# Optimization experiments

Hardware: AMD Instinct MI355X
Metric: run time of the kernel (lower is better)

Reference implementation:

```python
import jax, jax.numpy as jnp
import numpy as np
from jax import lax

L = 32          # lattice side
H = 128         # net_width / hidden_size
B = 512         # batch_size
EPS = 1e-8


def setup_inputs() -> dict:
    key = jax.random.key(0)
    k0, k1, k2, k3, k4 = jax.random.split(key, 5)
    # binary spin configurations in {0., 1.}
    samples = jnp.round(jax.random.uniform(k0, (B, L, L))).astype(jnp.float32)
    s1 = 1.0 / np.sqrt(H + 2)
    # per-cell linear1 weights: input = cat([x(2), h(H)]) -> H
    W1 = jax.random.uniform(k1, (L * L, H, H + 2), minval=-s1, maxval=s1, dtype=jnp.float32)
    b1 = jax.random.uniform(k2, (L * L, H), minval=-s1, maxval=s1, dtype=jnp.float32)
    sf = 1.0 / np.sqrt(H)
    # per-cell fc head: H -> 1
    Wf = jax.random.uniform(k3, (L * L, H), minval=-sf, maxval=sf, dtype=jnp.float32)
    bf = jax.random.uniform(k4, (L * L,), minval=-sf, maxval=sf, dtype=jnp.float32)
    return {"samples": samples, "W1": W1, "b1": b1, "Wf": Wf, "bf": bf}


def _log_prob(samples, W1, b1, Wf, bf):
    Bsz = samples.shape[0]
    dt = samples.dtype
    W1 = W1.reshape(L, L, H, H + 2)
    b1 = b1.reshape(L, L, H)
    Wf = Wf.reshape(L, L, H)
    bf = bf.reshape(L, L)

    rows = jnp.transpose(samples, (1, 0, 2))                       # (L, B, L)
    prev = jnp.concatenate([jnp.zeros((1, Bsz, L), dt), rows[:-1]], axis=0)  # row above (x_v); zeros for row 0
    parity = (jnp.arange(L) % 2) == 1                              # odd rows scan right-to-left (zigzag)

    def row_step(h_v, xs):
        cur, pv, p, Wr, br, wfr, bfr = xs
        # reorder everything into visitation order (reverse for odd rows)
        cur_o = jnp.where(p, cur[:, ::-1], cur)     # (B, L) current-row spins / mask
        pv_o = jnp.where(p, pv[:, ::-1], pv)        # (B, L) spins of row above (x_v)
        hv_o = jnp.where(p, h_v[::-1], h_v)         # (L, B, H) vertical hidden states
        Wr_o = jnp.where(p, Wr[::-1], Wr)
        br_o = jnp.where(p, br[::-1], br)
        wf_o = jnp.where(p, wfr[::-1], wfr)
        bf_o = jnp.where(p, bfr[::-1], bfr)
        # horizontal input x_h = previously visited spin in this row (0 at row start)
        xh = jnp.concatenate([jnp.zeros((Bsz, 1), dt), cur_o[:, :-1]], axis=1)  # (B, L)

        def cell(h_h, cxs):
            xh_j, xv_j, m_j, hv_j, W, b, wf, bfs = cxs
            xh_s = jnp.stack([xh_j, 1.0 - xh_j], axis=1)   # (B, 2)
            xv_s = jnp.stack([xv_j, 1.0 - xv_j], axis=1)   # (B, 2)
            # linear1 applied to both (x_h,h_h) and (x_v,h_v); linear2 is unused in the original forward
            inp = jnp.concatenate([xh_s, h_h], axis=1) + jnp.concatenate([xv_s, hv_j], axis=1)  # (B, H+2)
            h = jnp.tanh(inp @ W.T + 2.0 * b)              # (B, H)
            x_hat = jax.nn.sigmoid(h @ wf + bfs)           # (B,)
            lp = jnp.log(x_hat + EPS) * m_j + jnp.log(1.0 - x_hat + EPS) * (1.0 - m_j)
            return h, (h, lp)

        cxs = (xh.T, pv_o.T, cur_o.T, hv_o, Wr_o, br_o, wf_o, bf_o)
        _, (hs, lps) = lax.scan(cell, jnp.zeros((Bsz, H), dt), cxs)
        h_v_new = jnp.where(p, hs[::-1], hs)               # back to raw column order
        return h_v_new, lps.sum(axis=0)                    # (B,) row log-prob

    h_v0 = jnp.zeros((L, Bsz, H), dt)
    _, row_lps = lax.scan(row_step, h_v0, (rows, prev, parity, W1, b1, Wf, bf))
    return row_lps.sum(axis=0)                             # (B,)


def reference(samples, W1, b1, Wf, bf):
    return _log_prob(samples, W1, b1, Wf, bf)
```

## Files before the change

### kernel.cpp

```cpp
#include <hip/hip_runtime.h>
#include <math.h>
#include <stdint.h>

#define Lr 32
#define Hh 128
#define NCELL (Lr * Lr)
#define NEPS 1e-8f
#define CELLB 33792

typedef _Float16 f16;
typedef f16 h2 __attribute__((ext_vector_type(2)));
typedef uint32_t u32;
typedef u32 u32x4 __attribute__((ext_vector_type(4)));
typedef u32 u32x2 __attribute__((ext_vector_type(2)));

__device__ __forceinline__ void bar_lds() {
    asm volatile("s_waitcnt lgkmcnt(0)\n\ts_barrier" ::: "memory");
}

template<int CTRL>
__device__ __forceinline__ float dpp_get(float x) {
    return __int_as_float(__builtin_amdgcn_update_dpp(
        0, __float_as_int(x), CTRL, 0xf, 0xf, true));
}

__device__ __forceinline__ float rlane(float x, int l) {
    return __int_as_float(__builtin_amdgcn_readlane(__float_as_int(x), l));
}

__device__ __forceinline__ float dot2(h2 a, h2 b, float c) {
    return __builtin_amdgcn_fdot2(a, b, c, false);
}

__device__ __forceinline__ h2 bch2(u32 v) {
    union { u32 u; h2 h; } cv; cv.u = v; return cv.h;
}
__device__ __forceinline__ float h16(u32 w, int hi) {
    union { unsigned short u; f16 h; } c;
    c.u = (unsigned short)(hi ? (w >> 16) : (w & 0xffff));
    return (float)c.h;
}

__device__ __forceinline__ float fast_tanh(float x) {
    x = fminf(9.f, fmaxf(-9.f, x));
    const float e = __expf(2.f * x);
    return 1.f - 2.f / (e + 1.f);
}

__device__ __forceinline__ int cell_of(int s) {
    const int i = s >> 5, jj = s & 31;
    const int c = (i & 1) ? (Lr - 1 - jj) : jj;
    return i * Lr + c;
}

__global__ __launch_bounds__(256)
void transpose_w(const float* __restrict__ W1, const float* __restrict__ b1,
                 const float* __restrict__ Wf, char* __restrict__ Wt) {
    __shared__ float tile[Hh * 130];
    const int cell = blockIdx.x;
    const float* src = W1 + (size_t)cell * (Hh * 130);
    for (int idx = threadIdx.x; idx < Hh * 130; idx += 256)
        tile[idx] = src[idx];
    __syncthreads();
    char* dst = Wt + (size_t)cell * CELLB;
    const int t = threadIdx.x;
    for (int idx = t; idx < 2048; idx += 256) {
        const int c4 = idx >> 9, tt = idx & 511;
        const int kk = tt >> 2, q = tt & 3;
        union { u32x4 v; f16 h[8]; } o;
        for (int j = 0; j < 4; ++j) {
            const int p = q * 16 + c4 * 4 + j;
            o.h[2 * j]     = (f16)tile[kk * 130 + 2 + 2 * p];
            o.h[2 * j + 1] = (f16)tile[kk * 130 + 3 + 2 * p];
        }
        *(u32x4*)(dst + c4 * 8192 + tt * 16) = o.v;
    }
    if (t < Hh) {
        union { u32x2 v; f16 h[4]; } o;
        const float w0 = tile[t * 130 + 0], w1 = tile[t * 130 + 1];
        const float bb = 2.f * b1[cell * Hh + t];
        o.h[0] = (f16)(2.f * w1 + bb);
        o.h[1] = (f16)(w0 + w1 + bb);
        o.h[2] = (f16)(2.f * w0 + bb);
        o.h[3] = (f16)Wf[cell * Hh + t];
        *(u32x2*)(dst + 32768 + t * 8) = o.v;
    }
}

__global__ __launch_bounds__(512, 4)
void rnn2d(const float* __restrict__ samples,
           const char* __restrict__ Wt,
           const float* __restrict__ bfv,
           float* __restrict__ out)
{
    __shared__ __align__(16) h2  inp[2][64];
    __shared__ __align__(16) f16 hvh[Lr * Hh];
    __shared__ float smp[NCELL];
    __shared__ float bfs[NCELL];
    __shared__ __align__(16) float fp_[2][8];
    __shared__ int   sidx[2];
    __shared__ float lpb[2];

    const int t = threadIdx.x;
    const int k = t >> 2;
    const int q = t & 3;
    const int w = t >> 6;
    const int b = blockIdx.x;

    u32 vc[4], vt;
    for (int c4 = 0; c4 < 4; ++c4) vc[c4] = (u32)(c4 * 8192 + t * 16);
    vt = (u32)(32768 + k * 8);

    {
        f16* z1 = (f16*)inp;
        for (int idx = t; idx < 2 * 64 * 2; idx += 512) z1[idx] = (f16)0.f;
        f16* z2 = (f16*)hvh;
        for (int idx = t; idx < Lr * Hh; idx += 512) z2[idx] = (f16)0.f;
        for (int idx = t; idx < NCELL; idx += 512) {
            smp[idx] = samples[(size_t)b * NCELL + idx];
            bfs[idx] = bfv[idx];
        }
        if (t == 0) sidx[0] = 0;
    }
    float lp = 0.f;

    u32x4 A0,A1,A2,A3, B0,B1,B2,B3, C0,C1,C2,C3, D0,D1,D2,D3;
    u32x2 TA, TB, TC, TD;

#define ISSUE(S, W0,W1_,W2_,W3_, TT)                                        \
    {                                                                       \
        const int s_ = ((S) < NCELL) ? (S) : 0;   \
        const char* cb_ = Wt + (size_t)cell_of(s_) * CELLB;                 \
        asm volatile("global_load_dwordx4 %0, %1, %2" : "=v"(W0)  : "v"(vc[0]), "s"(cb_)); \
        asm volatile("global_load_dwordx4 %0, %1, %2" : "=v"(W1_) : "v"(vc[1]), "s"(cb_)); \
        asm volatile("global_load_dwordx4 %0, %1, %2" : "=v"(W2_) : "v"(vc[2]), "s"(cb_)); \
        asm volatile("global_load_dwordx4 %0, %1, %2" : "=v"(W3_) : "v"(vc[3]), "s"(cb_)); \
        asm volatile("global_load_dwordx2 %0, %1, %2" : "=v"(TT)  : "v"(vt),    "s"(cb_)); \
    }

#define WAITP()                                                             \
    asm volatile("s_waitcnt vmcnt(10)" ::: "memory");                       \
    __builtin_amdgcn_sched_barrier(0);

#define DOT4(WQ, QQ, C4)                                                    \
    {                                                                       \
        const u32x4 v_ = (WQ);                                              \
        const uint4 xa_ = *(const uint4*)&inp[QQ][q * 16 + (C4) * 4];       \
        a00 = dot2(bch2(v_.x), bch2(xa_.x), a00);                           \
        a01 = dot2(bch2(v_.y), bch2(xa_.y), a01);                           \
        a02 = dot2(bch2(v_.z), bch2(xa_.z), a02);                           \
        a03 = dot2(bch2(v_.w), bch2(xa_.w), a03);                           \
    }

#define PROC(S, Q, W0,W1_,W2_,W3_, TT)                                      \
    {                                                                       \
        const int i_ = (S) >> 5, j_ = (S) & 31;                             \
        const int c_ = (i_ & 1) ? (Lr - 1 - j_) : j_;                       \
        const int sn_ = ((S) + 1 < NCELL) ? (S) + 1 : (S);                  \
        const int in_ = sn_ >> 5, jn_ = sn_ & 31;                           \
        const int cn_ = (in_ & 1) ? (Lr - 1 - jn_) : jn_;                   \
        const float hvn = (float)hvh[cn_ * Hh + k];                         \
           \
                       \
        if (((t & 63) == 4) && (w == 4 || w == 5) && (S) > 0) {             \
            const int cp_ = cell_of((S) - 1);                               \
            const float4 fa_ = *(const float4*)&fp_[Q][0];                  \
            const float4 fb_ = *(const float4*)&fp_[Q][4];                  \
            const float z_ = ((fa_.x + fa_.y) + (fa_.z + fa_.w))            \
                           + ((fb_.x + fb_.y) + (fb_.z + fb_.w)) + bfs[cp_];\
            const float xh_ = 1.f / (1.f + __expf(-z_));                    \
            const float m_ = smp[cp_];                                      \
            lp += (w == 4) ? __logf(xh_ + NEPS) * m_                        \
                           : __logf(1.f - xh_ + NEPS) * (1.f - m_);         \
        }                                                                   \
           \
        float a00 = 0.f, a01 = 0.f, a02 = 0.f, a03 = 0.f;                   \
        DOT4(W0,  Q, 0) DOT4(W1_, Q, 1)                                     \
        DOT4(W2_, Q, 2) DOT4(W3_, Q, 3)                                     \
        float s0 = (a00 + a01) + (a02 + a03);                               \
        s0 += dpp_get<0xB1>(s0);                    \
        s0 += dpp_get<0x4E>(s0);   \
                     \
        const int sx = sidx[Q];                                             \
        const float t0_ = h16(TT.x, 0), t1_ = h16(TT.x, 1);                 \
        const float t2_ = h16(TT.y, 0), wfv = h16(TT.y, 1);                 \
        s0 += (sx == 2) ? t2_ : ((sx == 1) ? t1_ : t0_);                    \
        const float h0 = fast_tanh(s0);                                     \
            \
           \
        float f0 = h0 * wfv;                                                \
        f0 += dpp_get<0x141>(f0);                                           \
        f0 += dpp_get<0x140>(f0);                                           \
        f0 = f0 + rlane(f0, 16) + rlane(f0, 32) + rlane(f0, 48);            \
        if ((S) + 1 < NCELL) {                                              \
            const float v0 = ((jn_ == 0) ? 0.f : h0)                        \
                           + ((cn_ == c_) ? h0 : hvn);                      \
            const float v0p = __shfl_down(v0, 4);    \
            if ((t & 7) == 0) {                                             \
                h2 u0; u0.x = (f16)v0; u0.y = (f16)v0p;                     \
                inp[(Q) ^ 1][t >> 3] = u0;                                  \
            }                                                               \
            if (t == 0) {                                                   \
                const float xh0 = (jn_ == 0) ? 0.f : smp[i_ * Lr + c_];     \
                const float xv0 = (in_ == 0) ? 0.f                          \
                                             : smp[(in_ - 1) * Lr + cn_];   \
                sidx[(Q) ^ 1] = (int)(xh0 + xv0);                           \
            }                                                               \
        }                                                                   \
        if ((t & 3) == 0) hvh[c_ * Hh + k] = (f16)h0;    \
        if ((t & 63) == 0) fp_[(Q) ^ 1][w] = f0;                            \
        bar_lds();        \
    }

    ISSUE(0, A0,A1,A2,A3, TA);
    ISSUE(1, B0,B1,B2,B3, TB);
    __syncthreads();

    for (int s = 0; s < NCELL; s += 4) {
        ISSUE(s + 2, C0,C1,C2,C3, TC); WAITP();
        PROC(s,     0, A0,A1,A2,A3, TA);
        ISSUE(s + 3, D0,D1,D2,D3, TD); WAITP();
        PROC(s + 1, 1, B0,B1,B2,B3, TB);
        ISSUE(s + 4, A0,A1,A2,A3, TA); WAITP();
        PROC(s + 2, 0, C0,C1,C2,C3, TC);
        ISSUE(s + 5, B0,B1,B2,B3, TB); WAITP();
        PROC(s + 3, 1, D0,D1,D2,D3, TD);
    }
#undef ISSUE
#undef WAITP
#undef DOT4
#undef PROC

    if (((t & 63) == 4) && (w == 4 || w == 5)) {
        const int cp_ = cell_of(NCELL - 1);
        const float4 fa_ = *(const float4*)&fp_[0][0];
        const float4 fb_ = *(const float4*)&fp_[0][4];
        const float z_ = ((fa_.x + fa_.y) + (fa_.z + fa_.w))
                       + ((fb_.x + fb_.y) + (fb_.z + fb_.w)) + bfs[cp_];
        const float xh_ = 1.f / (1.f + __expf(-z_));
        const float m_ = smp[cp_];
        lp += (w == 4) ? __logf(xh_ + NEPS) * m_
                       : __logf(1.f - xh_ + NEPS) * (1.f - m_);
        lpb[w - 4] = lp;
    }
    __syncthreads();
    if (t == 0) out[b] = lpb[0] + lpb[1];
}

extern "C" void kernel_launch(void* const* d_in, const int* in_sizes, int n_in,
                              void* d_out, int out_size, void* d_ws, size_t ws_size,
                              hipStream_t stream) {
    const float* samples = (const float*)d_in[0];
    const float* W1      = (const float*)d_in[1];
    const float* b1      = (const float*)d_in[2];
    const float* Wf      = (const float*)d_in[3];
    const float* bf      = (const float*)d_in[4];
    float* outp = (float*)d_out;
    char* Wt = (char*)d_ws;

    transpose_w<<<1024, 256, 0, stream>>>(W1, b1, Wf, Wt);
    rnn2d<<<512, 512, 0, stream>>>(samples, Wt, bf, outp);
}
```

Baseline: 1.040 ms.

## Batch 16 samples per block and compute cell matvec with MFMA

The kernel used to run one block per sample, doing a 128x128 fp16 dot2 matvec per cell. Each block now handles 16 batch elements and computes the per-cell product as a 128x16 matrix multiply with 16x16x32 f16 MFMA instructions. Weights are re-laid out in the transpose kernel to match the MFMA A-operand fragments, and samples are bit-packed into per-cell masks. Each weight fetch is now reused across 16 samples, which cuts global weight traffic 16x. The cost is only 32 blocks, so far fewer CUs are busy and the serial chain of cells may become latency bound, and the per-element vertical hidden state takes a large LDS buffer.

Measured after the change: 1.222 ms. 1.17x slower.

```diff
diff --git a/kernel.cpp b/kernel.cpp
--- a/kernel.cpp
+++ b/kernel.cpp
@@ -7,46 +7,33 @@
 #define NCELL (Lr * Lr)
 #define NEPS 1e-8f
 #define CELLB 33792
+#define ELEMS 16
 
 typedef _Float16 f16;
-typedef f16 h2 __attribute__((ext_vector_type(2)));
+typedef f16 f16x4 __attribute__((ext_vector_type(4)));
+typedef f16 f16x8 __attribute__((ext_vector_type(8)));
+typedef float f32x4 __attribute__((ext_vector_type(4)));
 typedef uint32_t u32;
+typedef u32 u32x2 __attribute__((ext_vector_type(2)));
 typedef u32 u32x4 __attribute__((ext_vector_type(4)));
-typedef u32 u32x2 __attribute__((ext_vector_type(2)));
 
 __device__ __forceinline__ void bar_lds() {
     asm volatile("s_waitcnt lgkmcnt(0)\n\ts_barrier" ::: "memory");
 }
 
-template<int CTRL>
-__device__ __forceinline__ float dpp_get(float x) {
-    return __int_as_float(__builtin_amdgcn_update_dpp(
-        0, __float_as_int(x), CTRL, 0xf, 0xf, true));
-}
-
-__device__ __forceinline__ float rlane(float x, int l) {
-    return __int_as_float(__builtin_amdgcn_readlane(__float_as_int(x), l));
-}
-
-__device__ __forceinline__ float dot2(h2 a, h2 b, float c) {
-    return __builtin_amdgcn_fdot2(a, b, c, false);
-}
-
-__device__ __forceinline__ h2 bch2(u32 v) {
-    union { u32 u; h2 h; } cv; cv.u = v; return cv.h;
-}
-__device__ __forceinline__ float h16(u32 w, int hi) {
+__device__ __forceinline__ f16x8 asf16x8(u32x4 v) {
+    union { u32x4 u; f16x8 h; } c; c.u = v; return c.h;
+}
+__device__ __forceinline__ float h16(u32 wd, int hi) {
     union { unsigned short u; f16 h; } c;
-    c.u = (unsigned short)(hi ? (w >> 16) : (w & 0xffff));
+    c.u = (unsigned short)(hi ? (wd >> 16) : (wd & 0xffff));
     return (float)c.h;
 }
-
 __device__ __forceinline__ float fast_tanh(float x) {
     x = fminf(9.f, fmaxf(-9.f, x));
     const float e = __expf(2.f * x);
     return 1.f - 2.f / (e + 1.f);
 }
-
 __device__ __forceinline__ int cell_of(int s) {
     const int i = s >> 5, jj = s & 31;
     const int c = (i & 1) ? (Lr - 1 - jj) : jj;
@@ -59,192 +46,195 @@
     __shared__ float tile[Hh * 130];
     const int cell = blockIdx.x;
     const float* src = W1 + (size_t)cell * (Hh * 130);
-    for (int idx = threadIdx.x; idx < Hh * 130; idx += 256)
-        tile[idx] = src[idx];
+    for (int idx = threadIdx.x; idx < Hh * 130; idx += 256) tile[idx] = src[idx];
     __syncthreads();
     char* dst = Wt + (size_t)cell * CELLB;
-    const int t = threadIdx.x;
-    for (int idx = t; idx < 2048; idx += 256) {
-        const int c4 = idx >> 9, tt = idx & 511;
-        const int kk = tt >> 2, q = tt & 3;
+    for (int idx = threadIdx.x; idx < 2048; idx += 256) {
+        const int kw = idx >> 9, mt = (idx >> 6) & 7, l = idx & 63;
+        const int row = mt * 16 + (l & 15);
+        const int k0 = kw * 32 + (l >> 4) * 8;
         union { u32x4 v; f16 h[8]; } o;
-        for (int j = 0; j < 4; ++j) {
-            const int p = q * 16 + c4 * 4 + j;
-            o.h[2 * j]     = (f16)tile[kk * 130 + 2 + 2 * p];
-            o.h[2 * j + 1] = (f16)tile[kk * 130 + 3 + 2 * p];
-        }
-        *(u32x4*)(dst + c4 * 8192 + tt * 16) = o.v;
-    }
-    if (t < Hh) {
+        for (int j = 0; j < 8; ++j) o.h[j] = (f16)tile[row * 130 + 2 + k0 + j];
+        *(u32x4*)(dst + idx * 16) = o.v;
+    }
+    if (threadIdx.x < Hh) {
+        const int kk = threadIdx.x;
         union { u32x2 v; f16 h[4]; } o;
-        const float w0 = tile[t * 130 + 0], w1 = tile[t * 130 + 1];
-        const float bb = 2.f * b1[cell * Hh + t];
+        const float w0 = tile[kk * 130 + 0], w1 = tile[kk * 130 + 1];
+        const float bb = 2.f * b1[cell * Hh + kk];
         o.h[0] = (f16)(2.f * w1 + bb);
         o.h[1] = (f16)(w0 + w1 + bb);
         o.h[2] = (f16)(2.f * w0 + bb);
-        o.h[3] = (f16)Wf[cell * Hh + t];
-        *(u32x2*)(dst + 32768 + t * 8) = o.v;
-    }
-}
-
-__global__ __launch_bounds__(512, 4)
+        o.h[3] = (f16)Wf[cell * Hh + kk];
+        *(u32x2*)(dst + 32768 + kk * 8) = o.v;
+    }
+}
+
+__global__ __launch_bounds__(512, 2)
 void rnn2d(const float* __restrict__ samples,
            const char* __restrict__ Wt,
            const float* __restrict__ bfv,
            float* __restrict__ out)
 {
-    __shared__ __align__(16) h2  inp[2][64];
-    __shared__ __align__(16) f16 hvh[Lr * Hh];
-    __shared__ float smp[NCELL];
+    __shared__ __align__(16) f16 hvl[512 * 132];
+    __shared__ __align__(16) f16 inpL[2][ELEMS * 136];
+    __shared__ u32   smpw[NCELL];
     __shared__ float bfs[NCELL];
-    __shared__ __align__(16) float fp_[2][8];
-    __shared__ int   sidx[2];
-    __shared__ float lpb[2];
-
-    const int t = threadIdx.x;
-    const int k = t >> 2;
-    const int q = t & 3;
-    const int w = t >> 6;
-    const int b = blockIdx.x;
-
-    u32 vc[4], vt;
-    for (int c4 = 0; c4 < 4; ++c4) vc[c4] = (u32)(c4 * 8192 + t * 16);
-    vt = (u32)(32768 + k * 8);
+    __shared__ __align__(16) float fp_[2][ELEMS][8];
+
+    const int t  = threadIdx.x;
+    const int l  = t & 63;
+    const int w  = t >> 6;
+    const int e  = t & 15;
+    const int g  = (t >> 4) & 3;
+    const int b0 = blockIdx.x * ELEMS;
+
+    const u32 vc0 = (u32)(((0 * 8 + w) * 64 + l) * 16);
+    const u32 vc1 = (u32)(((1 * 8 + w) * 64 + l) * 16);
+    const u32 vc2 = (u32)(((2 * 8 + w) * 64 + l) * 16);
+    const u32 vc3 = (u32)(((3 * 8 + w) * 64 + l) * 16);
+    const u32 kq  = (u32)(w * 16 + g * 4);
+    const u32 vt0 = 32768 + kq * 8, vt1 = vt0 + 16;
 
     {
-        f16* z1 = (f16*)inp;
-        for (int idx = t; idx < 2 * 64 * 2; idx += 512) z1[idx] = (f16)0.f;
-        f16* z2 = (f16*)hvh;
-        for (int idx = t; idx < Lr * Hh; idx += 512) z2[idx] = (f16)0.f;
-        for (int idx = t; idx < NCELL; idx += 512) {
-            smp[idx] = samples[(size_t)b * NCELL + idx];
-            bfs[idx] = bfv[idx];
+        for (int c = 0; c < 33; ++c) *(f16x4*)&hvl[t * 132 + c * 4] = (f16x4)0;
+        u32* z = (u32*)inpL;
+        for (int idx = t; idx < 2176; idx += 512) z[idx] = 0;
+        if (t < 256) ((u32*)fp_)[t] = 0;
+        u32 w0 = 0, w1 = 0;
+        for (int ee = 0; ee < ELEMS; ++ee) {
+            w0 |= (samples[(size_t)(b0 + ee) * NCELL + t] != 0.f ? 1u : 0u) << ee;
+            w1 |= (samples[(size_t)(b0 + ee) * NCELL + t + 512] != 0.f ? 1u : 0u) << ee;
         }
-        if (t == 0) sidx[0] = 0;
+        smpw[t] = w0; smpw[t + 512] = w1;
+        bfs[t] = bfv[t]; bfs[t + 512] = bfv[t + 512];
     }
     float lp = 0.f;
+    __syncthreads();
 
     u32x4 A0,A1,A2,A3, B0,B1,B2,B3, C0,C1,C2,C3, D0,D1,D2,D3;
-    u32x2 TA, TB, TC, TD;
-
-#define ISSUE(S, W0,W1_,W2_,W3_, TT)                                        \
+    u32x4 AT0,AT1, BT0,BT1, CT0,CT1, DT0,DT1;
+
+#define ISSUE(S, R0,R1,R2,R3, T0,T1)                                        \
     {                                                                       \
-        const int s_ = ((S) < NCELL) ? (S) : 0;   \
+        const int s_ = ((S) < NCELL) ? (S) : 0;                             \
         const char* cb_ = Wt + (size_t)cell_of(s_) * CELLB;                 \
-        asm volatile("global_load_dwordx4 %0, %1, %2" : "=v"(W0)  : "v"(vc[0]), "s"(cb_)); \
-        asm volatile("global_load_dwordx4 %0, %1, %2" : "=v"(W1_) : "v"(vc[1]), "s"(cb_)); \
-        asm volatile("global_load_dwordx4 %0, %1, %2" : "=v"(W2_) : "v"(vc[2]), "s"(cb_)); \
-        asm volatile("global_load_dwordx4 %0, %1, %2" : "=v"(W3_) : "v"(vc[3]), "s"(cb_)); \
-        asm volatile("global_load_dwordx2 %0, %1, %2" : "=v"(TT)  : "v"(vt),    "s"(cb_)); \
+        asm volatile("global_load_dwordx4 %0, %1, %2" : "=v"(R0) : "v"(vc0), "s"(cb_)); \
+        asm volatile("global_load_dwordx4 %0, %1, %2" : "=v"(R1) : "v"(vc1), "s"(cb_)); \
+        asm volatile("global_load_dwordx4 %0, %1, %2" : "=v"(R2) : "v"(vc2), "s"(cb_)); \
+        asm volatile("global_load_dwordx4 %0, %1, %2" : "=v"(R3) : "v"(vc3), "s"(cb_)); \
+        asm volatile("global_load_dwordx4 %0, %1, %2" : "=v"(T0) : "v"(vt0), "s"(cb_)); \
+        asm volatile("global_load_dwordx4 %0, %1, %2" : "=v"(T1) : "v"(vt1), "s"(cb_)); \
     }
 
 #define WAITP()                                                             \
-    asm volatile("s_waitcnt vmcnt(10)" ::: "memory");                       \
+    asm volatile("s_waitcnt vmcnt(12)" ::: "memory");                       \
     __builtin_amdgcn_sched_barrier(0);
 
-#define DOT4(WQ, QQ, C4)                                                    \
-    {                                                                       \
-        const u32x4 v_ = (WQ);                                              \
-        const uint4 xa_ = *(const uint4*)&inp[QQ][q * 16 + (C4) * 4];       \
-        a00 = dot2(bch2(v_.x), bch2(xa_.x), a00);                           \
-        a01 = dot2(bch2(v_.y), bch2(xa_.y), a01);                           \
-        a02 = dot2(bch2(v_.z), bch2(xa_.z), a02);                           \
-        a03 = dot2(bch2(v_.w), bch2(xa_.w), a03);                           \
-    }
-
-#define PROC(S, Q, W0,W1_,W2_,W3_, TT)                                      \
+#define PROC(S, Q, R0,R1,R2,R3, T0,T1)                                      \
     {                                                                       \
         const int i_ = (S) >> 5, j_ = (S) & 31;                             \
         const int c_ = (i_ & 1) ? (Lr - 1 - j_) : j_;                       \
         const int sn_ = ((S) + 1 < NCELL) ? (S) + 1 : (S);                  \
         const int in_ = sn_ >> 5, jn_ = sn_ & 31;                           \
         const int cn_ = (in_ & 1) ? (Lr - 1 - jn_) : jn_;                   \
-        const float hvn = (float)hvh[cn_ * Hh + k];                         \
-           \
-                       \
-        if (((t & 63) == 4) && (w == 4 || w == 5) && (S) > 0) {             \
+          \
+        const f16x4 hvp = *(const f16x4*)&hvl[t * 132 + cn_ * 4];           \
+        \
+        if (w == 0 && l < 32 && (S) > 0) {                                  \
+            const int hf_ = l >> 4;                                         \
             const int cp_ = cell_of((S) - 1);                               \
-            const float4 fa_ = *(const float4*)&fp_[Q][0];                  \
-            const float4 fb_ = *(const float4*)&fp_[Q][4];                  \
+            const float4 fa_ = *(const float4*)&fp_[Q][e][0];               \
+            const float4 fb_ = *(const float4*)&fp_[Q][e][4];               \
             const float z_ = ((fa_.x + fa_.y) + (fa_.z + fa_.w))            \
                            + ((fb_.x + fb_.y) + (fb_.z + fb_.w)) + bfs[cp_];\
             const float xh_ = 1.f / (1.f + __expf(-z_));                    \
-            const float m_ = smp[cp_];                                      \
-            lp += (w == 4) ? __logf(xh_ + NEPS) * m_                        \
-                           : __logf(1.f - xh_ + NEPS) * (1.f - m_);         \
+            const float m_ = (float)((smpw[cp_] >> e) & 1);                 \
+            lp += (hf_ == 0) ? __logf(xh_ + NEPS) * m_                      \
+                             : __logf(1.f - xh_ + NEPS) * (1.f - m_);       \
         }                                                                   \
+               \
+        const int spv_ = (j_ > 0) ? cell_of((S)-1 >= 0 ? (S)-1 : 0) : 0;    \
+        const u32 wh_ = (j_ > 0) ? smpw[spv_] : 0u;                         \
+        const u32 wv_ = (i_ > 0) ? smpw[(i_ - 1) * Lr + c_] : 0u;           \
+        const int cse = (int)((wh_ >> e) & 1) + (int)((wv_ >> e) & 1);      \
+        const u32 q0l = T0.x, q0h = T0.y, q1l = T0.z, q1h = T0.w;           \
+        const u32 q2l = T1.x, q2h = T1.y, q3l = T1.z, q3h = T1.w;           \
+        const float ts0 = (cse==0)?h16(q0l,0):((cse==1)?h16(q0l,1):h16(q0h,0)); \
+        const float ts1 = (cse==0)?h16(q1l,0):((cse==1)?h16(q1l,1):h16(q1h,0)); \
+        const float ts2 = (cse==0)?h16(q2l,0):((cse==1)?h16(q2l,1):h16(q2h,0)); \
+        const float ts3 = (cse==0)?h16(q3l,0):((cse==1)?h16(q3l,1):h16(q3h,0)); \
+          \
+        const f16* ib_ = &inpL[Q][e * 136];                                 \
+        const f16x8 bq0 = *(const f16x8*)(ib_ +  0 + g * 8);                \
+        const f16x8 bq1 = *(const f16x8*)(ib_ + 32 + g * 8);                \
+        const f16x8 bq2 = *(const f16x8*)(ib_ + 64 + g * 8);                \
+        const f16x8 bq3 = *(const f16x8*)(ib_ + 96 + g * 8);                \
+        f32x4 accA; accA[0]=ts0; accA[1]=ts1; accA[2]=ts2; accA[3]=ts3;     \
+        f32x4 accB = (f32x4)0.f;                                            \
+        accA = __builtin_amdgcn_mfma_f32_16x16x32_f16(asf16x8(R0), bq0, accA, 0,0,0); \
+        accB = __builtin_amdgcn_mfma_f32_16x16x32_f16(asf16x8(R2), bq2, accB, 0,0,0); \
+        accA = __builtin_amdgcn_mfma_f32_16x16x32_f16(asf16x8(R1), bq1, accA, 0,0,0); \
+        accB = __builtin_amdgcn_mfma_f32_16x16x32_f16(asf16x8(R3), bq3, accB, 0,0,0); \
+        const f32x4 acc = accA + accB;                                      \
+        const float h0 = fast_tanh(acc[0]);                                 \
+        const float h1 = fast_tanh(acc[1]);                                 \
+        const float h2 = fast_tanh(acc[2]);                                 \
+        const float h3 = fast_tanh(acc[3]);                                 \
            \
-        float a00 = 0.f, a01 = 0.f, a02 = 0.f, a03 = 0.f;                   \
-        DOT4(W0,  Q, 0) DOT4(W1_, Q, 1)                                     \
-        DOT4(W2_, Q, 2) DOT4(W3_, Q, 3)                                     \
-        float s0 = (a00 + a01) + (a02 + a03);                               \
-        s0 += dpp_get<0xB1>(s0);                    \
-        s0 += dpp_get<0x4E>(s0);   \
-                     \
-        const int sx = sidx[Q];                                             \
-        const float t0_ = h16(TT.x, 0), t1_ = h16(TT.x, 1);                 \
-        const float t2_ = h16(TT.y, 0), wfv = h16(TT.y, 1);                 \
-        s0 += (sx == 2) ? t2_ : ((sx == 1) ? t1_ : t0_);                    \
-        const float h0 = fast_tanh(s0);                                     \
-            \
-           \
-        float f0 = h0 * wfv;                                                \
-        f0 += dpp_get<0x141>(f0);                                           \
-        f0 += dpp_get<0x140>(f0);                                           \
-        f0 = f0 + rlane(f0, 16) + rlane(f0, 32) + rlane(f0, 48);            \
+        float f_ = h0 * h16(q0h,1);                                         \
+        f_ = fmaf(h1, h16(q1h,1), f_);                                      \
+        f_ = fmaf(h2, h16(q2h,1), f_);                                      \
+        f_ = fmaf(h3, h16(q3h,1), f_);                                      \
+        f_ += __shfl_xor(f_, 16);                                           \
+        f_ += __shfl_xor(f_, 32);                                           \
+        if (l < 16) fp_[(Q) ^ 1][e][w] = f_;                                \
+                    \
         if ((S) + 1 < NCELL) {                                              \
-            const float v0 = ((jn_ == 0) ? 0.f : h0)                        \
-                           + ((cn_ == c_) ? h0 : hvn);                      \
-            const float v0p = __shfl_down(v0, 4);    \
-            if ((t & 7) == 0) {                                             \
-                h2 u0; u0.x = (f16)v0; u0.y = (f16)v0p;                     \
-                inp[(Q) ^ 1][t >> 3] = u0;                                  \
-            }                                                               \
-            if (t == 0) {                                                   \
-                const float xh0 = (jn_ == 0) ? 0.f : smp[i_ * Lr + c_];     \
-                const float xv0 = (in_ == 0) ? 0.f                          \
-                                             : smp[(in_ - 1) * Lr + cn_];   \
-                sidx[(Q) ^ 1] = (int)(xh0 + xv0);                           \
-            }                                                               \
+            const float hh_ = (jn_ == 0) ? 0.f : 1.f;                       \
+            const float v0 = hh_*h0 + ((cn_==c_) ? h0 : (float)hvp[0]);     \
+            const float v1 = hh_*h1 + ((cn_==c_) ? h1 : (float)hvp[1]);     \
+            const float v2 = hh_*h2 + ((cn_==c_) ? h2 : (float)hvp[2]);     \
+            const float v3 = hh_*h3 + ((cn_==c_) ? h3 : (float)hvp[3]);     \
+            f16x4 vp; vp[0]=(f16)v0; vp[1]=(f16)v1; vp[2]=(f16)v2; vp[3]=(f16)v3; \
+            *(f16x4*)&inpL[(Q) ^ 1][e * 136 + kq] = vp;                     \
         }                                                                   \
-        if ((t & 3) == 0) hvh[c_ * Hh + k] = (f16)h0;    \
-        if ((t & 63) == 0) fp_[(Q) ^ 1][w] = f0;                            \
-        bar_lds();        \
-    }
-
-    ISSUE(0, A0,A1,A2,A3, TA);
-    ISSUE(1, B0,B1,B2,B3, TB);
-    __syncthreads();
+        f16x4 hp; hp[0]=(f16)h0; hp[1]=(f16)h1; hp[2]=(f16)h2; hp[3]=(f16)h3; \
+        *(f16x4*)&hvl[t * 132 + c_ * 4] = hp;                               \
+        bar_lds();                    \
+    }
+
+    ISSUE(0, A0,A1,A2,A3, AT0,AT1);
+    ISSUE(1, B0,B1,B2,B3, BT0,BT1);
 
     for (int s = 0; s < NCELL; s += 4) {
-        ISSUE(s + 2, C0,C1,C2,C3, TC); WAITP();
-        PROC(s,     0, A0,A1,A2,A3, TA);
-        ISSUE(s + 3, D0,D1,D2,D3, TD); WAITP();
-        PROC(s + 1, 1, B0,B1,B2,B3, TB);
-        ISSUE(s + 4, A0,A1,A2,A3, TA); WAITP();
-        PROC(s + 2, 0, C0,C1,C2,C3, TC);
-        ISSUE(s + 5, B0,B1,B2,B3, TB); WAITP();
-        PROC(s + 3, 1, D0,D1,D2,D3, TD);
+        ISSUE(s + 2, C0,C1,C2,C3, CT0,CT1); WAITP();
+        PROC(s,     0, A0,A1,A2,A3, AT0,AT1);
+        ISSUE(s + 3, D0,D1,D2,D3, DT0,DT1); WAITP();
+        PROC(s + 1, 1, B0,B1,B2,B3, BT0,BT1);
+        ISSUE(s + 4, A0,A1,A2,A3, AT0,AT1); WAITP();
+        PROC(s + 2, 0, C0,C1,C2,C3, CT0,CT1);
+        ISSUE(s + 5, B0,B1,B2,B3, BT0,BT1); WAITP();
+        PROC(s + 3, 1, D0,D1,D2,D3, DT0,DT1);
     }
 #undef ISSUE
 #undef WAITP
-#undef DOT4
 #undef PROC
 
-    if (((t & 63) == 4) && (w == 4 || w == 5)) {
-        const int cp_ = cell_of(NCELL - 1);
-        const float4 fa_ = *(const float4*)&fp_[0][0];
-        const float4 fb_ = *(const float4*)&fp_[0][4];
-        const float z_ = ((fa_.x + fa_.y) + (fa_.z + fa_.w))
-                       + ((fb_.x + fb_.y) + (fb_.z + fb_.w)) + bfs[cp_];
-        const float xh_ = 1.f / (1.f + __expf(-z_));
-        const float m_ = smp[cp_];
-        lp += (w == 4) ? __logf(xh_ + NEPS) * m_
-                       : __logf(1.f - xh_ + NEPS) * (1.f - m_);
-        lpb[w - 4] = lp;
-    }
-    __syncthreads();
-    if (t == 0) out[b] = lpb[0] + lpb[1];
+    if (w == 0 && l < 32) {
+        const int hf = l >> 4;
+        const int cp = cell_of(NCELL - 1);
+        const float4 fa = *(const float4*)&fp_[0][e][0];
+        const float4 fb = *(const float4*)&fp_[0][e][4];
+        const float z = ((fa.x + fa.y) + (fa.z + fa.w))
+                      + ((fb.x + fb.y) + (fb.z + fb.w)) + bfs[cp];
+        const float xh = 1.f / (1.f + __expf(-z));
+        const float m = (float)((smpw[cp] >> e) & 1);
+        lp += (hf == 0) ? __logf(xh + NEPS) * m
+                        : __logf(1.f - xh + NEPS) * (1.f - m);
+        const float lpo = lp + __shfl_down(lp, 16);
+        if (hf == 0) out[b0 + e] = lpo;
+    }
 }
 
 extern "C" void kernel_launch(void* const* d_in, const int* in_sizes, int n_in,
@@ -259,5 +249,5 @@
     char* Wt = (char*)d_ws;
 
     transpose_w<<<1024, 256, 0, stream>>>(W1, b1, Wf, Wt);
-    rnn2d<<<512, 512, 0, stream>>>(samples, Wt, bf, outp);
-}
+    rnn2d<<<512 / ELEMS, 512, 0, stream>>>(samples, Wt, bf, outp);
+}
```
